# Performance work log

Hardware: AMD Instinct MI355X
Metric: run time of the kernel (lower is better)

Reference implementation:

```python
import jax, jax.numpy as jnp
import numpy as np
import math

B, T, D, H, FF, L, CS, LC = 8, 512, 512, 8, 2048, 6, 16, 4
DK = D // H
MIN16 = float(np.finfo(np.float16).min)  # masked_fill value used by the module


def _chunk_mask(size, ck, n_left):
    # subsequent_chunk_mask: row i attends [max((i//ck - n_left)*ck, 0), (i//ck + 1)*ck)
    i = np.arange(size)
    j = np.arange(size)
    ci = i // ck
    start = np.maximum((ci - n_left) * ck, 0)
    end = (ci + 1) * ck
    return (j[None, :] >= start[:, None]) & (j[None, :] < end[:, None])


def setup_inputs() -> dict:
    key = jax.random.key(0)
    ks = jax.random.split(key, 16)
    s = 0.02
    rn = lambda k, shp: jax.random.normal(k, shp, jnp.float32) * s
    xs = jax.random.normal(ks[0], (B, T, D), jnp.float32)
    # RelPositionalEncoding sinusoidal table
    pos = np.arange(T, dtype=np.float32)[:, None]
    div = np.exp(np.arange(0, D, 2, dtype=np.float32) * (-math.log(10000.0) / D))
    pe = np.zeros((T, D), np.float32)
    pe[:, 0::2] = np.sin(pos * div)
    pe[:, 1::2] = np.cos(pos * div)
    pos_emb = jnp.asarray(pe)[None]  # (1, T, D)
    mask = jnp.asarray(_chunk_mask(T, CS, LC))[None]  # (1, T, T) bool, True=attend
    return {
        'xs': xs, 'pos_emb': pos_emb, 'mask': mask,
        'Wq': rn(ks[1], (L, D, D)), 'bq': jnp.zeros((L, D)),
        'Wk': rn(ks[2], (L, D, D)), 'bk': jnp.zeros((L, D)),
        'Wv': rn(ks[3], (L, D, D)), 'bv': jnp.zeros((L, D)),
        'Wo': rn(ks[4], (L, D, D)), 'bo': jnp.zeros((L, D)),
        'Wp': rn(ks[5], (L, D, D)),
        'pbu': rn(ks[6], (L, H, DK)), 'pbv': rn(ks[7], (L, H, DK)),
        'ln1_s': jnp.ones((L, D)), 'ln1_b': jnp.zeros((L, D)),
        'ln2_s': jnp.ones((L, D)), 'ln2_b': jnp.zeros((L, D)),
        'W1': rn(ks[8], (L, D, FF)), 'b1': jnp.zeros((L, FF)),
        'W2': rn(ks[9], (L, FF, D)), 'b2': jnp.zeros((L, D)),
        'lnf_s': jnp.ones((D,)), 'lnf_b': jnp.zeros((D,)),
    }


def _ln(x, g, b):
    m = jnp.mean(x, -1, keepdims=True)
    v = jnp.var(x, -1, keepdims=True)
    return (x - m) * jax.lax.rsqrt(v + 1e-5) * g + b


def reference(xs, pos_emb, mask, Wq, bq, Wk, bk, Wv, bv, Wo, bo, Wp, pbu, pbv,
              ln1_s, ln1_b, ln2_s, ln2_b, W1, b1, W2, b2, lnf_s, lnf_b):
    x = xs * math.sqrt(D)          # xscale from positional encoding
    m = mask[:, None, :, :]        # (1,1,T,T)
    scale = 1.0 / math.sqrt(DK)
    for l in range(L):
        h = _ln(x, ln1_s[l], ln1_b[l])
        q = (h @ Wq[l] + bq[l]).reshape(B, T, H, DK)                       # (B,T,H,DK)
        k = (h @ Wk[l] + bk[l]).reshape(B, T, H, DK).transpose(0, 2, 1, 3)  # (B,H,T,DK)
        v = (h @ Wv[l] + bv[l]).reshape(B, T, H, DK).transpose(0, 2, 1, 3)
        p = (pos_emb @ Wp[l]).reshape(T, H, DK).transpose(1, 0, 2)          # (H,T,DK)
        qu = (q + pbu[l]).transpose(0, 2, 1, 3)  # (B,H,T,DK)
        qv = (q + pbv[l]).transpose(0, 2, 1, 3)
        ac = jnp.einsum('bhtd,bhsd->bhts', qu, k)
        bd = jnp.einsum('bhtd,hsd->bhts', qv, p)
        scores = jnp.where(m, (ac + bd) * scale, MIN16)
        attn = jnp.where(m, jax.nn.softmax(scores, axis=-1), 0.0)
        o = jnp.einsum('bhts,bhsd->bthd', attn, v).reshape(B, T, D)
        x = x + o @ Wo[l] + bo[l]
        h2 = _ln(x, ln2_s[l], ln2_b[l])
        x = x + jax.nn.relu(h2 @ W1[l] + b1[l]) @ W2[l] + b2[l]
    return _ln(x, lnf_s, lnf_b)
```

## Files before the change

### kernel.cpp

```cpp
#include <hip/hip_runtime.h>

#define B_ 8
#define T_ 512
#define D_ 512
#define H_ 8
#define FF_ 2048
#define L_ 6
#define CS_ 16
#define LC_ 4
#define DK_ 64
#define MT_ (B_*T_)

typedef unsigned short u16;
typedef __attribute__((ext_vector_type(8))) short bf8_t;
typedef __attribute__((ext_vector_type(4))) float f4_t;

__device__ __forceinline__ float bf2f(u16 u){
  union { unsigned int i; float f; } c; c.i = ((unsigned int)u) << 16; return c.f;
}
__device__ __forceinline__ u16 f2bf(float f){
  union { float f; unsigned int i; } c; c.f = f;
  unsigned int x = c.i;
  return (u16)((x + 0x7FFFu + ((x >> 16) & 1u)) >> 16);
}
__device__ __forceinline__ void ld_lds16(const u16* gp, u16* lp){
  __builtin_amdgcn_global_load_lds((const __attribute__((address_space(1))) void*)gp,
                                   (__attribute__((address_space(3))) void*)lp, 16, 0, 0);
}

__global__ void init_kernel(const float* __restrict__ xs, const float* __restrict__ pe,
                            float* __restrict__ x, u16* __restrict__ pe_bf)
{
  int stride = gridDim.x * blockDim.x;
  int i0 = blockIdx.x * blockDim.x + threadIdx.x;
  const float s = 22.62741699796952f;
  for (int i = i0; i < B_*T_*D_; i += stride) x[i] = xs[i] * s;
  for (int i = i0; i < T_*D_;    i += stride) pe_bf[i] = f2bf(pe[i]);
}

__global__ void transpose_kernel(const float* __restrict__ in, u16* __restrict__ out,
                                 int K, int N)
{
  __shared__ float tile[32][33];
  int l = blockIdx.z;
  const float* src = in + (size_t)l * K * N;
  u16* dst = out + (size_t)l * N * K;
  int n0 = blockIdx.x * 32, k0 = blockIdx.y * 32;
  int tx = threadIdx.x, ty = threadIdx.y;
  #pragma unroll
  for (int i = 0; i < 4; ++i)
    tile[ty + i*8][tx] = src[(size_t)(k0 + ty + i*8) * N + n0 + tx];
  __syncthreads();
  #pragma unroll
  for (int i = 0; i < 4; ++i)
    dst[(size_t)(n0 + ty + i*8) * K + k0 + tx] = f2bf(tile[tx][ty + i*8]);
}

__global__ void transpose_qkv_kernel(const float* __restrict__ Wq, const float* __restrict__ Wk,
                                     const float* __restrict__ Wv, u16* __restrict__ out)
{
  __shared__ float tile[32][33];
  int l = blockIdx.z;
  int n0 = blockIdx.x * 32, k0 = blockIdx.y * 32;
  const float* W = (n0 < 512) ? Wq : (n0 < 1024 ? Wk : Wv);
  int nn0 = n0 & 511;
  const float* src = W + (size_t)l * D_ * D_;
  u16* dst = out + (size_t)l * 3 * D_ * D_;
  int tx = threadIdx.x, ty = threadIdx.y;
  #pragma unroll
  for (int i = 0; i < 4; ++i)
    tile[ty + i*8][tx] = src[(size_t)(k0 + ty + i*8) * D_ + nn0 + tx];
  __syncthreads();
  #pragma unroll
  for (int i = 0; i < 4; ++i)
    dst[(size_t)(n0 + ty + i*8) * D_ + k0 + tx] = f2bf(tile[tx][ty + i*8]);
}

__global__ void pack_bias_kernel(const float* __restrict__ bq, const float* __restrict__ bk,
                                 const float* __restrict__ bv, float* __restrict__ out)
{
  int l = blockIdx.x, t = threadIdx.x;
  out[l*1536 + t]        = bq[l*512 + t];
  out[l*1536 + 512  + t] = bk[l*512 + t];
  out[l*1536 + 1024 + t] = bv[l*512 + t];
}

template <int OUTMODE>
__global__ __launch_bounds__(256) void ln_kernel(const float* __restrict__ x,
    const float* __restrict__ g, const float* __restrict__ b, void* __restrict__ outp)
{
  int lane = threadIdx.x & 63;
  int row  = (blockIdx.x << 2) + (threadIdx.x >> 6);
  const float* xr = x + (size_t)row * D_;
  int d = lane * 8;
  float4 a0 = *(const float4*)(xr + d);
  float4 a1 = *(const float4*)(xr + d + 4);
  float s  = a0.x+a0.y+a0.z+a0.w + a1.x+a1.y+a1.z+a1.w;
  float s2 = a0.x*a0.x+a0.y*a0.y+a0.z*a0.z+a0.w*a0.w
           + a1.x*a1.x+a1.y*a1.y+a1.z*a1.z+a1.w*a1.w;
  #pragma unroll
  for (int off = 32; off > 0; off >>= 1){ s += __shfl_xor(s, off); s2 += __shfl_xor(s2, off); }
  float m  = s * (1.0f / D_);
  float var = s2 * (1.0f / D_) - m*m;
  float rs = rsqrtf(var + 1e-5f);
  float4 g0 = *(const float4*)(g + d), g1 = *(const float4*)(g + d + 4);
  float4 b0 = *(const float4*)(b + d), b1 = *(const float4*)(b + d + 4);
  float o[8];
  o[0]=(a0.x-m)*rs*g0.x+b0.x; o[1]=(a0.y-m)*rs*g0.y+b0.y;
  o[2]=(a0.z-m)*rs*g0.z+b0.z; o[3]=(a0.w-m)*rs*g0.w+b0.w;
  o[4]=(a1.x-m)*rs*g1.x+b1.x; o[5]=(a1.y-m)*rs*g1.y+b1.y;
  o[6]=(a1.z-m)*rs*g1.z+b1.z; o[7]=(a1.w-m)*rs*g1.w+b1.w;
  if (OUTMODE == 1){
    float* outr = (float*)outp + (size_t)row * D_ + d;
    *(float4*)(outr)     = make_float4(o[0],o[1],o[2],o[3]);
    *(float4*)(outr + 4) = make_float4(o[4],o[5],o[6],o[7]);
  } else {
    u16* outr = (u16*)outp + (size_t)row * D_ + d;
    ushort4 w0, w1;
    w0.x=f2bf(o[0]); w0.y=f2bf(o[1]); w0.z=f2bf(o[2]); w0.w=f2bf(o[3]);
    w1.x=f2bf(o[4]); w1.y=f2bf(o[5]); w1.z=f2bf(o[6]); w1.w=f2bf(o[7]);
    *(ushort4*)(outr)     = w0;
    *(ushort4*)(outr + 4) = w1;
  }
}

template <int TN>
__global__ __launch_bounds__(256) void mgemm_kernel(
    const u16* __restrict__ A, const u16* __restrict__ Bt,
    const float* __restrict__ bias, const float* __restrict__ resid,
    void* __restrict__ C, int M, int N, int K,
    int relu, int bf16out, size_t wstride, size_t cstride)
{
  constexpr int NT = TN / 32;
  constexpr int SB = TN / 64;
  constexpr int S  = 2 + SB;
  Bt += (size_t)blockIdx.z * wstride;
  size_t coff = (size_t)blockIdx.z * cstride;

  __shared__ u16 As[2][128 * 32];
  __shared__ u16 Bs[2][TN * 32];

  int tid  = threadIdx.x;
  int wave = tid >> 6, lane = tid & 63;
  int wm = wave >> 1, wn = wave & 1;
  int fm = lane & 15, fq = lane >> 4;

  int m0 = blockIdx.y * 128, n0 = blockIdx.x * TN;

  f4_t acc[4][NT];
  #pragma unroll
  for (int i = 0; i < 4; ++i)
    #pragma unroll
    for (int j = 0; j < NT; ++j) acc[i][j] = (f4_t)0.0f;

  int srow = lane >> 2;
  int selem = (lane & 3) << 3;

  auto stage = [&](int bufi, int k0){
    #pragma unroll
    for (int j = 0; j < 2; ++j){
      int c = wave * 2 + j;
      ld_lds16(A + (size_t)(m0 + c*16 + srow) * K + k0 + selem, &As[bufi][c * 512]);
    }
    #pragma unroll
    for (int j = 0; j < SB; ++j){
      int c = wave * SB + j;
      ld_lds16(Bt + (size_t)(n0 + c*16 + srow) * K + k0 + selem, &Bs[bufi][c * 512]);
    }
  };

  stage(0, 0);
  int buf = 0;
  for (int k0 = 0; k0 < K; k0 += 32){
    if (k0 + 32 < K){
      stage(buf ^ 1, k0 + 32);
      asm volatile("s_waitcnt vmcnt(%0)" :: "n"(S) : "memory");
    } else {
      asm volatile("s_waitcnt vmcnt(0)" ::: "memory");
    }
    asm volatile("s_barrier" ::: "memory");

    bf8_t af[4], bfr[NT];
    #pragma unroll
    for (int mi = 0; mi < 4; ++mi)
      af[mi] = *(const bf8_t*)&As[buf][(wm*64 + mi*16 + fm) * 32 + fq*8];
    #pragma unroll
    for (int nj = 0; nj < NT; ++nj)
      bfr[nj] = *(const bf8_t*)&Bs[buf][(wn*(TN/2) + nj*16 + fm) * 32 + fq*8];
    #pragma unroll
    for (int mi = 0; mi < 4; ++mi)
      #pragma unroll
      for (int nj = 0; nj < NT; ++nj)
        acc[mi][nj] = __builtin_amdgcn_mfma_f32_16x16x32_bf16(af[mi], bfr[nj], acc[mi][nj], 0, 0, 0);

    asm volatile("s_barrier" ::: "memory");
    buf ^= 1;
  }

  int rbase = m0 + wm*64, cbase = n0 + wn*(TN/2);
  #pragma unroll
  for (int mi = 0; mi < 4; ++mi){
    #pragma unroll
    for (int nj = 0; nj < NT; ++nj){
      int col = cbase + nj*16 + fm;
      float bia = bias ? bias[col] : 0.0f;
      #pragma unroll
      for (int r = 0; r < 4; ++r){
        int row = rbase + mi*16 + fq*4 + r;
        size_t idx = coff + (size_t)row * N + col;
        float val = acc[mi][nj][r] + bia;
        if (relu)  val = fmaxf(val, 0.0f);
        if (resid) val += resid[idx];
        if (bf16out) ((u16*)C)[idx] = f2bf(val);
        else         ((float*)C)[idx] = val;
      }
    }
  }
}

__global__ __launch_bounds__(64) void attn_kernel(
    const u16* __restrict__ qkv, const u16* __restrict__ p,
    const float* __restrict__ pbu, const float* __restrict__ pbv,
    u16* __restrict__ o)
{
  int ci = blockIdx.x, h = blockIdx.y, b = blockIdx.z;
  int t0 = ci * CS_;
  int cb = ci - LC_; if (cb < 0) cb = 0;
  int c0 = cb * CS_;
  int ncol = (ci + 1) * CS_ - c0;

  __shared__ u16 smem[15648];
  u16* qu = smem;
  u16* qv = smem + 1024;
  u16* kp = smem + 2048;
  u16* pp = smem + 2048 + 5120;
  float* vf  = (float*)(smem + 2048);
  float* psf = (float*)(smem + 12288);

  int lane = threadIdx.x;
  int fm = lane & 15, fq = lane >> 4;

  const u16* kbase = qkv + ((size_t)(b*T_ + c0)) * 1536 + 512 + h*DK_;
  const u16* pbase = p + (size_t)c0 * D_ + h*DK_;
  int srow8 = lane >> 3, scol = (lane & 7) << 3;
  #pragma unroll
  for (int c = 0; c < 10; ++c){
    ld_lds16(kbase + (size_t)(c*8 + srow8) * 1536 + scol, kp + c*512);
    ld_lds16(pbase + (size_t)(c*8 + srow8) * D_   + scol, pp + c*512);
  }
  const u16* qbase = qkv + ((size_t)(b*T_ + t0)) * 1536 + h*DK_;
  #pragma unroll
  for (int it = 0; it < 4; ++it){
    int i = it*256 + lane*4; int r = i >> 6; int d = i & 63;
    ushort4 w = *(const ushort4*)(qbase + (size_t)r * 1536 + d);
    float4 bu = *(const float4*)(pbu + h*DK_ + d);
    float4 bv = *(const float4*)(pbv + h*DK_ + d);
    ushort4 ou, ov;
    ou.x = f2bf(bf2f(w.x) + bu.x); ou.y = f2bf(bf2f(w.y) + bu.y);
    ou.z = f2bf(bf2f(w.z) + bu.z); ou.w = f2bf(bf2f(w.w) + bu.w);
    ov.x = f2bf(bf2f(w.x) + bv.x); ov.y = f2bf(bf2f(w.y) + bv.y);
    ov.z = f2bf(bf2f(w.z) + bv.z); ov.w = f2bf(bf2f(w.w) + bv.w);
    *(ushort4*)(qu + r*64 + d) = ou;
    *(ushort4*)(qv + r*64 + d) = ov;
  }
  __syncthreads();

  bf8_t au0 = *(const bf8_t*)(qu + fm*64 + fq*8);
  bf8_t au1 = *(const bf8_t*)(qu + fm*64 + 32 + fq*8);
  bf8_t av0 = *(const bf8_t*)(qv + fm*64 + fq*8);
  bf8_t av1 = *(const bf8_t*)(qv + fm*64 + 32 + fq*8);
  f4_t acc[5];
  #pragma unroll
  for (int nt = 0; nt < 5; ++nt) acc[nt] = (f4_t)0.0f;
  #pragma unroll
  for (int nt = 0; nt < 5; ++nt){
    const u16* kr = kp + (nt*16 + fm)*64;
    const u16* pr = pp + (nt*16 + fm)*64;
    bf8_t bk0 = *(const bf8_t*)(kr + fq*8);
    bf8_t bk1 = *(const bf8_t*)(kr + 32 + fq*8);
    bf8_t bp0 = *(const bf8_t*)(pr + fq*8);
    bf8_t bp1 = *(const bf8_t*)(pr + 32 + fq*8);
    f4_t a = acc[nt];
    a = __builtin_amdgcn_mfma_f32_16x16x32_bf16(au0, bk0, a, 0, 0, 0);
    a = __builtin_amdgcn_mfma_f32_16x16x32_bf16(au1, bk1, a, 0, 0, 0);
    a = __builtin_amdgcn_mfma_f32_16x16x32_bf16(av0, bp0, a, 0, 0, 0);
    a = __builtin_amdgcn_mfma_f32_16x16x32_bf16(av1, bp1, a, 0, 0, 0);
    acc[nt] = a;
  }

  const float scale = 0.125f;
  float mx[4], sm[4];
  float e[5][4];
  #pragma unroll
  for (int r = 0; r < 4; ++r) mx[r] = -3.0e38f;
  #pragma unroll
  for (int nt = 0; nt < 5; ++nt){
    bool valid = (nt*16 + fm) < ncol;
    #pragma unroll
    for (int r = 0; r < 4; ++r){
      float v = valid ? acc[nt][r] : -3.0e38f;
      mx[r] = fmaxf(mx[r], v);
    }
  }
  #pragma unroll
  for (int r = 0; r < 4; ++r){
    #pragma unroll
    for (int m = 1; m < 16; m <<= 1) mx[r] = fmaxf(mx[r], __shfl_xor(mx[r], m));
    sm[r] = 0.0f;
  }
  #pragma unroll
  for (int nt = 0; nt < 5; ++nt){
    bool valid = (nt*16 + fm) < ncol;
    #pragma unroll
    for (int r = 0; r < 4; ++r){
      float ev = valid ? __expf((acc[nt][r] - mx[r]) * scale) : 0.0f;
      e[nt][r] = ev; sm[r] += ev;
    }
  }
  #pragma unroll
  for (int r = 0; r < 4; ++r){
    #pragma unroll
    for (int m = 1; m < 16; m <<= 1) sm[r] += __shfl_xor(sm[r], m);
    sm[r] = 1.0f / sm[r];
  }
  #pragma unroll
  for (int nt = 0; nt < 5; ++nt)
    #pragma unroll
    for (int r = 0; r < 4; ++r)
      psf[(fq*4 + r)*105 + nt*16 + fm] = e[nt][r] * sm[r];
  __syncthreads();

  const u16* vbase = qkv + ((size_t)(b*T_ + c0)) * 1536 + 1024 + h*DK_;
  #pragma unroll
  for (int it = 0; it < 20; ++it){
    int i = it*256 + lane*4; int s = i >> 6; int d = i & 63;
    ushort4 w = *(const ushort4*)(vbase + (size_t)s * 1536 + d);
    float4 f; f.x = bf2f(w.x); f.y = bf2f(w.y); f.z = bf2f(w.z); f.w = bf2f(w.w);
    *(float4*)(vf + s*64 + d) = f;
  }
  __syncthreads();

  float oacc[16];
  #pragma unroll
  for (int ii = 0; ii < 16; ++ii) oacc[ii] = 0.0f;
  const float* psr = psf + fm*105;
  const float* vcol = vf + fq*16;
  for (int s = 0; s < 80; ++s){
    float pv = psr[s];
    const float* vr = vcol + s*64;
    float4 v0 = *(const float4*)(vr);
    float4 v1 = *(const float4*)(vr + 4);
    float4 v2 = *(const float4*)(vr + 8);
    float4 v3 = *(const float4*)(vr + 12);
    oacc[0]  += pv*v0.x; oacc[1]  += pv*v0.y; oacc[2]  += pv*v0.z; oacc[3]  += pv*v0.w;
    oacc[4]  += pv*v1.x; oacc[5]  += pv*v1.y; oacc[6]  += pv*v1.z; oacc[7]  += pv*v1.w;
    oacc[8]  += pv*v2.x; oacc[9]  += pv*v2.y; oacc[10] += pv*v2.z; oacc[11] += pv*v2.w;
    oacc[12] += pv*v3.x; oacc[13] += pv*v3.y; oacc[14] += pv*v3.z; oacc[15] += pv*v3.w;
  }
  u16* ob = o + ((size_t)(b*T_ + t0 + fm)) * D_ + h*DK_ + fq*16;
  #pragma unroll
  for (int q4 = 0; q4 < 4; ++q4){
    ushort4 w;
    w.x = f2bf(oacc[q4*4+0]); w.y = f2bf(oacc[q4*4+1]);
    w.z = f2bf(oacc[q4*4+2]); w.w = f2bf(oacc[q4*4+3]);
    *(ushort4*)(ob + q4*4) = w;
  }
}

extern "C" void kernel_launch(void* const* d_in, const int* in_sizes, int n_in,
                              void* d_out, int out_size, void* d_ws, size_t ws_size,
                              hipStream_t stream)
{
  int s0 = (n_in >= 24) ? 0 : -1;
  const float* xs   = (const float*)d_in[0];
  const float* pe   = (const float*)d_in[1];
  const float* Wq   = (const float*)d_in[3  + s0];
  const float* bq   = (const float*)d_in[4  + s0];
  const float* Wk   = (const float*)d_in[5  + s0];
  const float* bk   = (const float*)d_in[6  + s0];
  const float* Wv   = (const float*)d_in[7  + s0];
  const float* bv   = (const float*)d_in[8  + s0];
  const float* Wo   = (const float*)d_in[9  + s0];
  const float* bo   = (const float*)d_in[10 + s0];
  const float* Wp   = (const float*)d_in[11 + s0];
  const float* pbu  = (const float*)d_in[12 + s0];
  const float* pbv  = (const float*)d_in[13 + s0];
  const float* ln1s = (const float*)d_in[14 + s0];
  const float* ln1b = (const float*)d_in[15 + s0];
  const float* ln2s = (const float*)d_in[16 + s0];
  const float* ln2b = (const float*)d_in[17 + s0];
  const float* W1   = (const float*)d_in[18 + s0];
  const float* b1   = (const float*)d_in[19 + s0];
  const float* W2   = (const float*)d_in[20 + s0];
  const float* b2   = (const float*)d_in[21 + s0];
  const float* lnfs = (const float*)d_in[22 + s0];
  const float* lnfb = (const float*)d_in[23 + s0];

  float* ws = (float*)d_ws;
  size_t cur = 0;
  float* x      = ws + cur;            cur += (size_t)MT_*D_;
  u16*   region = (u16*)(ws + cur);    cur += (size_t)MT_*FF_/2;
  u16*   qkv_bf = region;
  u16*   ff_bf  = region;
  u16*   h_bf   = (u16*)(ws + cur);    cur += (size_t)MT_*D_/2;
  u16*   ob_bf  = (u16*)(ws + cur);    cur += (size_t)MT_*D_/2;
  u16*   pe_bf  = (u16*)(ws + cur);    cur += (size_t)T_*D_/2;
  u16*   pbuf   = (u16*)(ws + cur);    cur += (size_t)L_*T_*D_/2;
  u16*   qkvt   = (u16*)(ws + cur);    cur += (size_t)L_*3*D_*D_/2;
  u16*   wot    = (u16*)(ws + cur);    cur += (size_t)L_*D_*D_/2;
  u16*   w1t    = (u16*)(ws + cur);    cur += (size_t)L_*D_*FF_/2;
  u16*   w2t    = (u16*)(ws + cur);    cur += (size_t)L_*FF_*D_/2;
  u16*   wpt    = (u16*)(ws + cur);    cur += (size_t)L_*D_*D_/2;
  float* bqkv   = ws + cur;            cur += (size_t)L_*3*D_;

  dim3 tb(32, 8);
  transpose_qkv_kernel<<<dim3(48, 16, L_), tb, 0, stream>>>(Wq, Wk, Wv, qkvt);
  transpose_kernel<<<dim3(16, 16, L_), tb, 0, stream>>>(Wo, wot, D_, D_);
  transpose_kernel<<<dim3(64, 16, L_), tb, 0, stream>>>(W1, w1t, D_, FF_);
  transpose_kernel<<<dim3(16, 64, L_), tb, 0, stream>>>(W2, w2t, FF_, D_);
  transpose_kernel<<<dim3(16, 16, L_), tb, 0, stream>>>(Wp, wpt, D_, D_);
  pack_bias_kernel<<<dim3(L_), dim3(512), 0, stream>>>(bq, bk, bv, bqkv);
  init_kernel<<<dim3(512), dim3(256), 0, stream>>>(xs, pe, x, pe_bf);

  dim3 blk(256);
  mgemm_kernel<64><<<dim3(8, 4, L_), blk, 0, stream>>>(
      pe_bf, wpt, nullptr, nullptr, pbuf, T_, D_, D_, 0, 1,
      (size_t)D_*D_, (size_t)T_*D_);

  for (int l = 0; l < L_; ++l){
    ln_kernel<0><<<dim3(MT_/4), blk, 0, stream>>>(x, ln1s + l*D_, ln1b + l*D_, h_bf);
    mgemm_kernel<128><<<dim3(12, 32, 1), blk, 0, stream>>>(
        h_bf, qkvt + (size_t)l*3*D_*D_, bqkv + l*3*D_, nullptr, qkv_bf,
        MT_, 3*D_, D_, 0, 1, 0, 0);
    attn_kernel<<<dim3(T_/CS_, H_, B_), dim3(64), 0, stream>>>(
        qkv_bf, pbuf + (size_t)l*T_*D_, pbu + l*H_*DK_, pbv + l*H_*DK_, ob_bf);
    mgemm_kernel<64><<<dim3(8, 32, 1), blk, 0, stream>>>(
        ob_bf, wot + (size_t)l*D_*D_, bo + l*D_, x, x, MT_, D_, D_, 0, 0, 0, 0);
    ln_kernel<0><<<dim3(MT_/4), blk, 0, stream>>>(x, ln2s + l*D_, ln2b + l*D_, h_bf);
    mgemm_kernel<128><<<dim3(16, 32, 1), blk, 0, stream>>>(
        h_bf, w1t + (size_t)l*D_*FF_, b1 + l*FF_, nullptr, ff_bf,
        MT_, FF_, D_, 1, 1, 0, 0);
    mgemm_kernel<64><<<dim3(8, 32, 1), blk, 0, stream>>>(
        ff_bf, w2t + (size_t)l*FF_*D_, b2 + l*D_, x, x, MT_, D_, FF_, 0, 0, 0, 0);
  }
  ln_kernel<1><<<dim3(MT_/4), blk, 0, stream>>>(x, lnfs, lnfb, d_out);
}
```

Baseline: 978.6 us.

## Use split-K with atomic residual accumulation, triple buffering, and fixed 64-wide tiles

The GEMM kernel is fixed at a 128x64 tile and moves from double to triple buffering, issuing loads two K-steps ahead. The Wo and W2 projections (N=512) now use split-K over 2 and 4 chunks, with each chunk atomically adding its partial sum into the fp32 residual x. This fills more of the GPU for those narrow GEMMs. The QKV and W1 GEMMs shrink from 128 to 64 columns per tile, which doubles their block count but lowers data reuse per tile, and the atomics add contention and nondeterministic summation order.

```diff
diff --git a/kernel.cpp b/kernel.cpp
--- a/kernel.cpp
+++ b/kernel.cpp
@@ -124,21 +124,24 @@
   }
 }
 
-template <int TN>
 __global__ __launch_bounds__(256) void mgemm_kernel(
     const u16* __restrict__ A, const u16* __restrict__ Bt,
     const float* __restrict__ bias, const float* __restrict__ resid,
     void* __restrict__ C, int M, int N, int K,
-    int relu, int bf16out, size_t wstride, size_t cstride)
-{
-  constexpr int NT = TN / 32;
-  constexpr int SB = TN / 64;
-  constexpr int S  = 2 + SB;
-  Bt += (size_t)blockIdx.z * wstride;
-  size_t coff = (size_t)blockIdx.z * cstride;
-
-  __shared__ u16 As[2][128 * 32];
-  __shared__ u16 Bs[2][TN * 32];
+    int relu, int bf16out, size_t wstride, size_t cstride, int kchunk)
+{
+  constexpr int TN = 64, NT = 2, S = 3;
+  size_t coff = 0;
+  int kbeg = 0, kend = K;
+  if (kchunk > 0){
+    kbeg = blockIdx.z * kchunk; kend = kbeg + kchunk;
+  } else {
+    Bt += (size_t)blockIdx.z * wstride;
+    coff = (size_t)blockIdx.z * cstride;
+  }
+
+  __shared__ u16 As[3][128 * 32];
+  __shared__ u16 Bs[3][TN * 32];
 
   int tid  = threadIdx.x;
   int wave = tid >> 6, lane = tid & 63;
@@ -162,18 +165,17 @@
       int c = wave * 2 + j;
       ld_lds16(A + (size_t)(m0 + c*16 + srow) * K + k0 + selem, &As[bufi][c * 512]);
     }
-    #pragma unroll
-    for (int j = 0; j < SB; ++j){
-      int c = wave * SB + j;
-      ld_lds16(Bt + (size_t)(n0 + c*16 + srow) * K + k0 + selem, &Bs[bufi][c * 512]);
-    }
+    ld_lds16(Bt + (size_t)(n0 + wave*16 + srow) * K + k0 + selem, &Bs[bufi][wave * 512]);
   };
 
-  stage(0, 0);
+  stage(0, kbeg);
+  if (kbeg + 32 < kend) stage(1, kbeg + 32);
   int buf = 0;
-  for (int k0 = 0; k0 < K; k0 += 32){
-    if (k0 + 32 < K){
-      stage(buf ^ 1, k0 + 32);
+  for (int k0 = kbeg; k0 < kend; k0 += 32){
+    if (k0 + 64 < kend){
+      stage((buf + 2) % 3, k0 + 64);
+      asm volatile("s_waitcnt vmcnt(%0)" :: "n"(2*S) : "memory");
+    } else if (k0 + 32 < kend){
       asm volatile("s_waitcnt vmcnt(%0)" :: "n"(S) : "memory");
     } else {
       asm volatile("s_waitcnt vmcnt(0)" ::: "memory");
@@ -186,7 +188,7 @@
       af[mi] = *(const bf8_t*)&As[buf][(wm*64 + mi*16 + fm) * 32 + fq*8];
     #pragma unroll
     for (int nj = 0; nj < NT; ++nj)
-      bfr[nj] = *(const bf8_t*)&Bs[buf][(wn*(TN/2) + nj*16 + fm) * 32 + fq*8];
+      bfr[nj] = *(const bf8_t*)&Bs[buf][(wn*32 + nj*16 + fm) * 32 + fq*8];
     #pragma unroll
     for (int mi = 0; mi < 4; ++mi)
       #pragma unroll
@@ -194,25 +196,42 @@
         acc[mi][nj] = __builtin_amdgcn_mfma_f32_16x16x32_bf16(af[mi], bfr[nj], acc[mi][nj], 0, 0, 0);
 
     asm volatile("s_barrier" ::: "memory");
-    buf ^= 1;
-  }
-
-  int rbase = m0 + wm*64, cbase = n0 + wn*(TN/2);
-  #pragma unroll
-  for (int mi = 0; mi < 4; ++mi){
-    #pragma unroll
-    for (int nj = 0; nj < NT; ++nj){
-      int col = cbase + nj*16 + fm;
-      float bia = bias ? bias[col] : 0.0f;
+    buf = (buf + 1) % 3;
+  }
+
+  int rbase = m0 + wm*64, cbase = n0 + wn*32;
+  if (kchunk > 0){
+    int addb = (blockIdx.z == 0) && bias;
+    #pragma unroll
+    for (int mi = 0; mi < 4; ++mi){
       #pragma unroll
-      for (int r = 0; r < 4; ++r){
-        int row = rbase + mi*16 + fq*4 + r;
-        size_t idx = coff + (size_t)row * N + col;
-        float val = acc[mi][nj][r] + bia;
-        if (relu)  val = fmaxf(val, 0.0f);
-        if (resid) val += resid[idx];
-        if (bf16out) ((u16*)C)[idx] = f2bf(val);
-        else         ((float*)C)[idx] = val;
+      for (int nj = 0; nj < NT; ++nj){
+        int col = cbase + nj*16 + fm;
+        float bia = addb ? bias[col] : 0.0f;
+        #pragma unroll
+        for (int r = 0; r < 4; ++r){
+          int row = rbase + mi*16 + fq*4 + r;
+          atomicAdd((float*)C + (size_t)row * N + col, acc[mi][nj][r] + bia);
+        }
+      }
+    }
+  } else {
+    #pragma unroll
+    for (int mi = 0; mi < 4; ++mi){
+      #pragma unroll
+      for (int nj = 0; nj < NT; ++nj){
+        int col = cbase + nj*16 + fm;
+        float bia = bias ? bias[col] : 0.0f;
+        #pragma unroll
+        for (int r = 0; r < 4; ++r){
+          int row = rbase + mi*16 + fq*4 + r;
+          size_t idx = coff + (size_t)row * N + col;
+          float val = acc[mi][nj][r] + bia;
+          if (relu)  val = fmaxf(val, 0.0f);
+          if (resid) val += resid[idx];
+          if (bf16out) ((u16*)C)[idx] = f2bf(val);
+          else         ((float*)C)[idx] = val;
+        }
       }
     }
   }
@@ -423,25 +442,27 @@
   init_kernel<<<dim3(512), dim3(256), 0, stream>>>(xs, pe, x, pe_bf);
 
   dim3 blk(256);
-  mgemm_kernel<64><<<dim3(8, 4, L_), blk, 0, stream>>>(
+  mgemm_kernel<<<dim3(8, 4, L_), blk, 0, stream>>>(
       pe_bf, wpt, nullptr, nullptr, pbuf, T_, D_, D_, 0, 1,
-      (size_t)D_*D_, (size_t)T_*D_);
+      (size_t)D_*D_, (size_t)T_*D_, 0);
 
   for (int l = 0; l < L_; ++l){
     ln_kernel<0><<<dim3(MT_/4), blk, 0, stream>>>(x, ln1s + l*D_, ln1b + l*D_, h_bf);
-    mgemm_kernel<128><<<dim3(12, 32, 1), blk, 0, stream>>>(
+    mgemm_kernel<<<dim3(24, 32, 1), blk, 0, stream>>>(
         h_bf, qkvt + (size_t)l*3*D_*D_, bqkv + l*3*D_, nullptr, qkv_bf,
-        MT_, 3*D_, D_, 0, 1, 0, 0);
+        MT_, 3*D_, D_, 0, 1, 0, 0, 0);
     attn_kernel<<<dim3(T_/CS_, H_, B_), dim3(64), 0, stream>>>(
         qkv_bf, pbuf + (size_t)l*T_*D_, pbu + l*H_*DK_, pbv + l*H_*DK_, ob_bf);
-    mgemm_kernel<64><<<dim3(8, 32, 1), blk, 0, stream>>>(
-        ob_bf, wot + (size_t)l*D_*D_, bo + l*D_, x, x, MT_, D_, D_, 0, 0, 0, 0);
+    mgemm_kernel<<<dim3(8, 32, 2), blk, 0, stream>>>(
+        ob_bf, wot + (size_t)l*D_*D_, bo + l*D_, nullptr, x,
+        MT_, D_, D_, 0, 0, 0, 0, 256);
     ln_kernel<0><<<dim3(MT_/4), blk, 0, stream>>>(x, ln2s + l*D_, ln2b + l*D_, h_bf);
-    mgemm_kernel<128><<<dim3(16, 32, 1), blk, 0, stream>>>(
+    mgemm_kernel<<<dim3(32, 32, 1), blk, 0, stream>>>(
         h_bf, w1t + (size_t)l*D_*FF_, b1 + l*FF_, nullptr, ff_bf,
-        MT_, FF_, D_, 1, 1, 0, 0);
-    mgemm_kernel<64><<<dim3(8, 32, 1), blk, 0, stream>>>(
-        ff_bf, w2t + (size_t)l*FF_*D_, b2 + l*D_, x, x, MT_, D_, FF_, 0, 0, 0, 0);
+        MT_, FF_, D_, 1, 1, 0, 0, 0);
+    mgemm_kernel<<<dim3(8, 32, 4), blk, 0, stream>>>(
+        ff_bf, w2t + (size_t)l*FF_*D_, b2 + l*D_, nullptr, x,
+        MT_, D_, FF_, 0, 0, 0, 0, 512);
   }
   ln_kernel<1><<<dim3(MT_/4), blk, 0, stream>>>(x, lnfs, lnfb, d_out);
 }
```

Measured after the change: 971.1 us. About the same (-0.8%).
